# Performance work log

Hardware: AMD Instinct MI355X
Metric: run time of the kernel (lower is better)

Reference implementation:

```python
import jax, jax.numpy as jnp
import numpy as np

EPSILON = 1e-15
LOG2 = 0.6931471805599453
N_VARS = 4096
BATCH = 512
OUT_SIZES = [16384, 8192, 4096, 2048]
FANINS = [4, 2, 4, 2]


def log1mexp(x):
    # accurate log(1 - exp(x)) for x < 0
    return jnp.where(x > -LOG2,
                     jnp.log(-jnp.expm1(x)),
                     jnp.log1p(-jnp.exp(x)))


def encode_input(pos):
    # rows: [-inf, 0, pos0, neg0, pos1, neg1, ...]
    neg = log1mexp(pos)
    inter = jnp.stack([pos, neg], axis=1).reshape(2 * pos.shape[0], pos.shape[1])
    head = jnp.stack([jnp.full(pos.shape[1:], -jnp.inf, pos.dtype),
                      jnp.zeros(pos.shape[1:], pos.dtype)])
    return jnp.concatenate([head, inter], axis=0)


def product_layer(x, ptrs, seg, n_out):
    return jax.ops.segment_sum(x[ptrs], seg, num_segments=n_out)


def sum_layer(x, ptrs, seg, n_out):
    g = x[ptrs]
    a = jax.lax.stop_gradient(jax.ops.segment_max(g, seg, num_segments=n_out))
    s = jax.ops.segment_sum(jnp.exp(g - a[seg]), seg, num_segments=n_out)
    return jnp.log(s + EPSILON) + a


def setup_inputs() -> dict:
    rng = np.random.default_rng(0)
    # log-probabilities in (-inf, 0): pos = log(u), u in (0,1)
    u = rng.uniform(1e-4, 1.0 - 1e-4, size=(N_VARS, BATCH)).astype(np.float32)
    x = jnp.asarray(np.log(u))

    inputs = {"x": x}
    prev_size = 2 * N_VARS + 2
    for i, (n_out, fanin) in enumerate(zip(OUT_SIZES, FANINS)):
        n_edges = n_out * fanin
        lo = 1 if i == 0 else 0  # avoid the -inf constant row at layer 0
        ptrs = rng.integers(lo, prev_size, size=n_edges).astype(np.int64)
        seg = np.repeat(np.arange(n_out, dtype=np.int64), fanin)
        inputs[f"ptrs{i}"] = jnp.asarray(ptrs)
        inputs[f"seg{i}"] = jnp.asarray(seg)
        prev_size = n_out
    return inputs


def reference(x, ptrs0, seg0, ptrs1, seg1, ptrs2, seg2, ptrs3, seg3):
    h = encode_input(x)
    ptrs = [ptrs0, ptrs1, ptrs2, ptrs3]
    segs = [seg0, seg1, seg2, seg3]
    for i, n_out in enumerate(OUT_SIZES):
        if i % 2 == 0:
            h = product_layer(h, ptrs[i], segs[i], n_out)
        else:
            h = sum_layer(h, ptrs[i], segs[i], n_out)
    return h
```

## Files before the change

### kernel.cpp

```cpp
#include <hip/hip_runtime.h>
#include <math.h>

#define BATCH    512
#define N_VARS   4096
#define H_ROWS   (2 * N_VARS + 2)
#define N_OUT1   8192
#define N_OUT3   2048
#define TPB      1024
#define SMEM_BYTES (H_ROWS * sizeof(float2))

__device__ __forceinline__ float log1mexp_fast(float x) {
    return __logf(1.0f - __expf(x));
}

__device__ __forceinline__ float2 lse2_fast2(float2 a, float2 b) {
    float2 r;
    float mx = fmaxf(a.x, b.x), my = fmaxf(a.y, b.y);
    r.x = mx + __logf(1.0f + __expf(-fabsf(a.x - b.x)));
    r.y = my + __logf(1.0f + __expf(-fabsf(a.y - b.y)));
    return r;
}

__global__ void build_tabs_kernel(const int* __restrict__ p0,
                                  const int* __restrict__ p1,
                                  const int* __restrict__ p2,
                                  const int* __restrict__ p3,
                                  int4* __restrict__ tabB,
                                  int4* __restrict__ tabC) {
    int o = blockIdx.x * blockDim.x + threadIdx.x;
    if (o < N_OUT1) {
        int2 pp = ((const int2*)p1)[o];
        tabB[2 * o]     = ((const int4*)p0)[pp.x];
        tabB[2 * o + 1] = ((const int4*)p0)[pp.y];
    } else {
        int oc = o - N_OUT1;
        int2 pp = ((const int2*)p3)[oc];
        tabC[2 * oc]     = ((const int4*)p2)[pp.x];
        tabC[2 * oc + 1] = ((const int4*)p2)[pp.y];
    }
}

#define TDIM 32
__global__ void transpose_kernel(const float* __restrict__ in,
                                 float* __restrict__ out, int R, int C) {
    __shared__ float tile[TDIM][TDIM + 1];
    int cb = blockIdx.x * TDIM;
    int rb = blockIdx.y * TDIM;
    int tx = threadIdx.x, ty = threadIdx.y;
#pragma unroll
    for (int j = 0; j < TDIM; j += 8)
        tile[ty + j][tx] = in[(size_t)(rb + ty + j) * C + cb + tx];
    __syncthreads();
#pragma unroll
    for (int j = 0; j < TDIM; j += 8)
        out[(size_t)(cb + ty + j) * R + rb + tx] = tile[tx][ty + j];
}

__global__ void __launch_bounds__(TPB, 4)
fused_spn_kernel(const float* __restrict__ xT,
                 const int4* __restrict__ tabB,
                 const int4* __restrict__ tabC,
                 float* __restrict__ outT) {
    extern __shared__ float2 buf[];
    const int b0 = 2 * blockIdx.x;
    const int b1 = b0 + 1;
    const int t = threadIdx.x;

    if (t == 0) {
        buf[0] = make_float2(-INFINITY, -INFINITY);
        buf[1] = make_float2(0.f, 0.f);
    }
    {
        float4 pa = ((const float4*)(xT + (size_t)b0 * N_VARS))[t];
        float4 pb = ((const float4*)(xT + (size_t)b1 * N_VARS))[t];
        int base = 8 * t + 2;
        buf[base + 0] = make_float2(pa.x, pb.x);
        buf[base + 1] = make_float2(log1mexp_fast(pa.x), log1mexp_fast(pb.x));
        buf[base + 2] = make_float2(pa.y, pb.y);
        buf[base + 3] = make_float2(log1mexp_fast(pa.y), log1mexp_fast(pb.y));
        buf[base + 4] = make_float2(pa.z, pb.z);
        buf[base + 5] = make_float2(log1mexp_fast(pa.z), log1mexp_fast(pb.z));
        buf[base + 6] = make_float2(pa.w, pb.w);
        buf[base + 7] = make_float2(log1mexp_fast(pa.w), log1mexp_fast(pb.w));
    }
    __syncthreads();

    float2 r1[N_OUT1 / TPB];
#pragma unroll
    for (int c = 0; c < N_OUT1 / TPB; c += 4) {
        int4 qa[4], qb[4];
#pragma unroll
        for (int k = 0; k < 4; ++k) {
            int o = t + (c + k) * TPB;
            qa[k] = tabB[2 * o];
            qb[k] = tabB[2 * o + 1];
        }
#pragma unroll
        for (int k = 0; k < 4; ++k) {
            float2 va0 = buf[qa[k].x], va1 = buf[qa[k].y];
            float2 va2 = buf[qa[k].z], va3 = buf[qa[k].w];
            float2 vb0 = buf[qb[k].x], vb1 = buf[qb[k].y];
            float2 vb2 = buf[qb[k].z], vb3 = buf[qb[k].w];
            float2 ga = make_float2(va0.x + va1.x + va2.x + va3.x,
                                    va0.y + va1.y + va2.y + va3.y);
            float2 gb = make_float2(vb0.x + vb1.x + vb2.x + vb3.x,
                                    vb0.y + vb1.y + vb2.y + vb3.y);
            r1[c + k] = lse2_fast2(ga, gb);
        }
    }
    __syncthreads();
#pragma unroll
    for (int k = 0; k < N_OUT1 / TPB; ++k)
        buf[t + k * TPB] = r1[k];
    __syncthreads();

    {
        int4 qa[2], qb[2];
#pragma unroll
        for (int k = 0; k < 2; ++k) {
            int o = t + k * TPB;
            qa[k] = tabC[2 * o];
            qb[k] = tabC[2 * o + 1];
        }
#pragma unroll
        for (int k = 0; k < 2; ++k) {
            int o = t + k * TPB;
            float2 va0 = buf[qa[k].x], va1 = buf[qa[k].y];
            float2 va2 = buf[qa[k].z], va3 = buf[qa[k].w];
            float2 vb0 = buf[qb[k].x], vb1 = buf[qb[k].y];
            float2 vb2 = buf[qb[k].z], vb3 = buf[qb[k].w];
            float2 ga = make_float2(va0.x + va1.x + va2.x + va3.x,
                                    va0.y + va1.y + va2.y + va3.y);
            float2 gb = make_float2(vb0.x + vb1.x + vb2.x + vb3.x,
                                    vb0.y + vb1.y + vb2.y + vb3.y);
            float2 r = lse2_fast2(ga, gb);
            outT[(size_t)b0 * N_OUT3 + o] = r.x;
            outT[(size_t)b1 * N_OUT3 + o] = r.y;
        }
    }
}

extern "C" void kernel_launch(void* const* d_in, const int* in_sizes, int n_in,
                              void* d_out, int out_size, void* d_ws, size_t ws_size,
                              hipStream_t stream) {
    const float* x     = (const float*)d_in[0];
    const int*   ptrs0 = (const int*)d_in[1];
    const int*   ptrs1 = (const int*)d_in[3];
    const int*   ptrs2 = (const int*)d_in[5];
    const int*   ptrs3 = (const int*)d_in[7];
    float* out = (float*)d_out;

    float* xT   = (float*)d_ws;
    float* outT = xT + (size_t)N_VARS * BATCH;
    int4*  tabB = (int4*)(outT + (size_t)N_OUT3 * BATCH);
    int4*  tabC = tabB + 2 * N_OUT1;

    static bool attr_set = false;
    if (!attr_set) {
        hipFuncSetAttribute((const void*)fused_spn_kernel,
                            hipFuncAttributeMaxDynamicSharedMemorySize, SMEM_BYTES);
        attr_set = true;
    }

    build_tabs_kernel<<<(N_OUT1 + N_OUT3) / 256, 256, 0, stream>>>(
        ptrs0, ptrs1, ptrs2, ptrs3, tabB, tabC);

    transpose_kernel<<<dim3(BATCH / TDIM, N_VARS / TDIM), dim3(32, 8), 0, stream>>>(
        x, xT, N_VARS, BATCH);

    fused_spn_kernel<<<BATCH / 2, TPB, SMEM_BYTES, stream>>>(xT, tabB, tabC, outT);

    transpose_kernel<<<dim3(N_OUT3 / TDIM, BATCH / TDIM), dim3(32, 8), 0, stream>>>(
        outT, out, BATCH, N_OUT3);
}
```

Measured before the change: 91.74 us.

## Drop transpose kernels and read/write batch-major data directly in fused kernel

Removes the input and output transpose kernels. Each block now reads its pair of batch columns as strided float2 loads straight from x and writes float2 results straight into the final output layout. This saves two kernel launches and a round trip through workspace, at the cost of uncoalesced 8-byte strided global accesses. hipFuncSetAttribute is now called on every launch instead of once.

```diff
diff --git a/kernel.cpp b/kernel.cpp
--- a/kernel.cpp
+++ b/kernel.cpp
@@ -15,9 +15,8 @@
 
 __device__ __forceinline__ float2 lse2_fast2(float2 a, float2 b) {
     float2 r;
-    float mx = fmaxf(a.x, b.x), my = fmaxf(a.y, b.y);
-    r.x = mx + __logf(1.0f + __expf(-fabsf(a.x - b.x)));
-    r.y = my + __logf(1.0f + __expf(-fabsf(a.y - b.y)));
+    r.x = fmaxf(a.x, b.x) + __logf(1.0f + __expf(-fabsf(a.x - b.x)));
+    r.y = fmaxf(a.y, b.y) + __logf(1.0f + __expf(-fabsf(a.y - b.y)));
     return r;
 }
 
@@ -40,48 +39,26 @@
     }
 }
 
-#define TDIM 32
-__global__ void transpose_kernel(const float* __restrict__ in,
-                                 float* __restrict__ out, int R, int C) {
-    __shared__ float tile[TDIM][TDIM + 1];
-    int cb = blockIdx.x * TDIM;
-    int rb = blockIdx.y * TDIM;
-    int tx = threadIdx.x, ty = threadIdx.y;
-#pragma unroll
-    for (int j = 0; j < TDIM; j += 8)
-        tile[ty + j][tx] = in[(size_t)(rb + ty + j) * C + cb + tx];
-    __syncthreads();
-#pragma unroll
-    for (int j = 0; j < TDIM; j += 8)
-        out[(size_t)(cb + ty + j) * R + rb + tx] = tile[tx][ty + j];
-}
-
 __global__ void __launch_bounds__(TPB, 4)
-fused_spn_kernel(const float* __restrict__ xT,
+fused_spn_kernel(const float* __restrict__ x,
                  const int4* __restrict__ tabB,
                  const int4* __restrict__ tabC,
-                 float* __restrict__ outT) {
+                 float* __restrict__ out) {
     extern __shared__ float2 buf[];
-    const int b0 = 2 * blockIdx.x;
-    const int b1 = b0 + 1;
+    const int bp = blockIdx.x;
     const int t = threadIdx.x;
+    const float2* x2 = (const float2*)x;
 
     if (t == 0) {
         buf[0] = make_float2(-INFINITY, -INFINITY);
         buf[1] = make_float2(0.f, 0.f);
     }
-    {
-        float4 pa = ((const float4*)(xT + (size_t)b0 * N_VARS))[t];
-        float4 pb = ((const float4*)(xT + (size_t)b1 * N_VARS))[t];
-        int base = 8 * t + 2;
-        buf[base + 0] = make_float2(pa.x, pb.x);
-        buf[base + 1] = make_float2(log1mexp_fast(pa.x), log1mexp_fast(pb.x));
-        buf[base + 2] = make_float2(pa.y, pb.y);
-        buf[base + 3] = make_float2(log1mexp_fast(pa.y), log1mexp_fast(pb.y));
-        buf[base + 4] = make_float2(pa.z, pb.z);
-        buf[base + 5] = make_float2(log1mexp_fast(pa.z), log1mexp_fast(pb.z));
-        buf[base + 6] = make_float2(pa.w, pb.w);
-        buf[base + 7] = make_float2(log1mexp_fast(pa.w), log1mexp_fast(pb.w));
+#pragma unroll
+    for (int k = 0; k < N_VARS / TPB; ++k) {
+        int i = t + k * TPB;
+        float2 p = x2[(size_t)i * (BATCH / 2) + bp];
+        buf[2 * i + 2] = p;
+        buf[2 * i + 3] = make_float2(log1mexp_fast(p.x), log1mexp_fast(p.y));
     }
     __syncthreads();
 
@@ -133,9 +110,7 @@
                                     va0.y + va1.y + va2.y + va3.y);
             float2 gb = make_float2(vb0.x + vb1.x + vb2.x + vb3.x,
                                     vb0.y + vb1.y + vb2.y + vb3.y);
-            float2 r = lse2_fast2(ga, gb);
-            outT[(size_t)b0 * N_OUT3 + o] = r.x;
-            outT[(size_t)b1 * N_OUT3 + o] = r.y;
+            ((float2*)(out + (size_t)o * BATCH))[bp] = lse2_fast2(ga, gb);
         }
     }
 }
@@ -150,26 +125,14 @@
     const int*   ptrs3 = (const int*)d_in[7];
     float* out = (float*)d_out;
 
-    float* xT   = (float*)d_ws;
-    float* outT = xT + (size_t)N_VARS * BATCH;
-    int4*  tabB = (int4*)(outT + (size_t)N_OUT3 * BATCH);
-    int4*  tabC = tabB + 2 * N_OUT1;
+    int4* tabB = (int4*)d_ws;
+    int4* tabC = tabB + 2 * N_OUT1;
 
-    static bool attr_set = false;
-    if (!attr_set) {
-        hipFuncSetAttribute((const void*)fused_spn_kernel,
-                            hipFuncAttributeMaxDynamicSharedMemorySize, SMEM_BYTES);
-        attr_set = true;
-    }
+    hipFuncSetAttribute((const void*)fused_spn_kernel,
+                        hipFuncAttributeMaxDynamicSharedMemorySize, SMEM_BYTES);
 
     build_tabs_kernel<<<(N_OUT1 + N_OUT3) / 256, 256, 0, stream>>>(
         ptrs0, ptrs1, ptrs2, ptrs3, tabB, tabC);
 
-    transpose_kernel<<<dim3(BATCH / TDIM, N_VARS / TDIM), dim3(32, 8), 0, stream>>>(
-        x, xT, N_VARS, BATCH);
-
-    fused_spn_kernel<<<BATCH / 2, TPB, SMEM_BYTES, stream>>>(xT, tabB, tabC, outT);
-
-    transpose_kernel<<<dim3(N_OUT3 / TDIM, BATCH / TDIM), dim3(32, 8), 0, stream>>>(
-        outT, out, BATCH, N_OUT3);
+    fused_spn_kernel<<<BATCH / 2, TPB, SMEM_BYTES, stream>>>(x, tabB, tabC, out);
 }
```

New measurement: 94.73 us. 1.03x slower.
